# Kernel tuning notes

Hardware: AMD Instinct MI355X
Metric: run time of the kernel (lower is better)

Reference implementation:

```python
import jax, jax.numpy as jnp
import numpy as np

CELL_DIM = 64
FIELD_SIZE = 1.0

def setup_inputs() -> dict:
    key = jax.random.key(0)
    k1, k2 = jax.random.split(key)
    x = jax.random.normal(k1, (8192, CELL_DIM), dtype=jnp.float32)
    placeCells = jax.random.normal(k2, (512, CELL_DIM), dtype=jnp.float32)
    return {"x": x, "placeCells": placeCells}

def reference(x, placeCells):
    # states: (N, cellDim)
    states = x.reshape(-1, CELL_DIM)
    # broadcast L1 distance to every codebook cell: (N, numCells)
    l1 = jnp.sum(jnp.abs(states[:, None, :] - placeCells[None, :, :]), axis=-1)
    dists_squared = l1 * l1
    unnormalized = -dists_squared / (2.0 * FIELD_SIZE * FIELD_SIZE)
    return jax.nn.softmax(unnormalized, axis=1)
```

## Files before the change

### kernel.cpp

```cpp
#include <hip/hip_runtime.h>

#define DIM    64
#define NCELLS 512
#define CHUNK  256
#define KHALF  32
#define ROWS_PER_BLOCK 8
#define NROWS  8192

__global__ __launch_bounds__(256, 4)
void placecells_kernel(const float* __restrict__ x,
                       const float* __restrict__ pc,
                       float* __restrict__ out)
{
    __shared__ float pcT[KHALF * CHUNK];

    const int tid = (int)threadIdx.x;
    const int l   = tid & 63;
    const int w   = __builtin_amdgcn_readfirstlane(tid >> 6);
    const int rowBase = (int)blockIdx.x * ROWS_PER_BLOCK + w * 2;

    float4 a00{0,0,0,0}, a01{0,0,0,0};
    float4 a10{0,0,0,0}, a11{0,0,0,0};

    auto do_phase = [&](int ch, int h, float4& A0, float4& A1) {
        #pragma unroll
        for (int it = 0; it < 8; ++it) {
            int idx = it * 256 + tid;
            int cl  = idx >> 3;
            int kq  = idx & 7;
            float4 v = *(const float4*)(pc + (ch * CHUNK + cl) * DIM + h * KHALF + kq * 4);
            int k4g = h * 8 + kq;
            int pq  = (cl >> 2) ^ k4g;
            float* p = &pcT[(kq * 4) * CHUNK + pq * 4 + (cl & 3)];
            p[0 * CHUNK] = v.x;
            p[1 * CHUNK] = v.y;
            p[2 * CHUNK] = v.z;
            p[3 * CHUNK] = v.w;
        }
        __syncthreads();

        #pragma unroll
        for (int kq = 0; kq < 8; ++kq) {
            const int k4g = h * 8 + kq;
            float4 xv0 = *(const float4*)(x + (rowBase + 0) * DIM + h * KHALF + kq * 4);
            float4 xv1 = *(const float4*)(x + (rowBase + 1) * DIM + h * KHALF + kq * 4);
            const int pq4 = (l ^ k4g) * 4;
            #pragma unroll
            for (int j = 0; j < 4; ++j) {
                float4 pv = *(const float4*)(&pcT[(kq * 4 + j) * CHUNK + pq4]);
                float x0 = (j == 0) ? xv0.x : (j == 1) ? xv0.y : (j == 2) ? xv0.z : xv0.w;
                float x1 = (j == 0) ? xv1.x : (j == 1) ? xv1.y : (j == 2) ? xv1.z : xv1.w;
                A0.x += fabsf(x0 - pv.x); A0.y += fabsf(x0 - pv.y);
                A0.z += fabsf(x0 - pv.z); A0.w += fabsf(x0 - pv.w);
                A1.x += fabsf(x1 - pv.x); A1.y += fabsf(x1 - pv.y);
                A1.z += fabsf(x1 - pv.z); A1.w += fabsf(x1 - pv.w);
            }
        }
        __syncthreads();
    };

    do_phase(0, 0, a00, a10);
    do_phase(0, 1, a00, a10);
    do_phase(1, 0, a01, a11);
    do_phase(1, 1, a01, a11);

    auto finish_row = [&](float4 a, float4 b, int r) {
        float mn = fminf(fminf(fminf(a.x, a.y), fminf(a.z, a.w)),
                         fminf(fminf(b.x, b.y), fminf(b.z, b.w)));
        #pragma unroll
        for (int off = 32; off > 0; off >>= 1)
            mn = fminf(mn, __shfl_xor(mn, off, 64));
        float m2 = mn * mn;

        float e0 = __expf(0.5f * (m2 - a.x * a.x));
        float e1 = __expf(0.5f * (m2 - a.y * a.y));
        float e2 = __expf(0.5f * (m2 - a.z * a.z));
        float e3 = __expf(0.5f * (m2 - a.w * a.w));
        float e4 = __expf(0.5f * (m2 - b.x * b.x));
        float e5 = __expf(0.5f * (m2 - b.y * b.y));
        float e6 = __expf(0.5f * (m2 - b.z * b.z));
        float e7 = __expf(0.5f * (m2 - b.w * b.w));
        float s = ((e0 + e1) + (e2 + e3)) + ((e4 + e5) + (e6 + e7));
        #pragma unroll
        for (int off = 32; off > 0; off >>= 1)
            s += __shfl_xor(s, off, 64);
        float inv = 1.0f / s;

        float* orow = out + (size_t)(rowBase + r) * NCELLS;
        *(float4*)(orow + 4 * l)         = make_float4(e0 * inv, e1 * inv, e2 * inv, e3 * inv);
        *(float4*)(orow + CHUNK + 4 * l) = make_float4(e4 * inv, e5 * inv, e6 * inv, e7 * inv);
    };
    finish_row(a00, a01, 0);
    finish_row(a10, a11, 1);
}

extern "C" void kernel_launch(void* const* d_in, const int* in_sizes, int n_in,
                              void* d_out, int out_size, void* d_ws, size_t ws_size,
                              hipStream_t stream)
{
    const float* x  = (const float*)d_in[0];
    const float* pc = (const float*)d_in[1];
    float* out = (float*)d_out;
    placecells_kernel<<<dim3(NROWS / ROWS_PER_BLOCK), dim3(256), 0, stream>>>(x, pc, out);
}
```

Baseline: 80.37 us.

## Stage the whole place-cell codebook in LDS once per 1024-thread block

Each block now uses 1024 threads covering 32 rows and copies the full 512x64 codebook (128 KB) into dynamic LDS in one transposed, XOR-swizzled pass. This replaces the four chunk/half phases and their extra barriers. The goal is to cut the repeated LDS refills of the codebook per row and the synchronisation between phases. In exchange, the large LDS footprint allows only one block per CU and leaves no overlap between the load and the compute. It also keeps __launch_bounds__(1024,4), which may squeeze the register budget and cause spills.

After: 79.04 us. Within noise of the previous version (-1.6%).

```diff
diff --git a/kernel.cpp b/kernel.cpp
--- a/kernel.cpp
+++ b/kernel.cpp
@@ -2,67 +2,62 @@
 
 #define DIM    64
 #define NCELLS 512
-#define CHUNK  256
-#define KHALF  32
-#define ROWS_PER_BLOCK 8
+#define ROWS_PER_BLOCK 32
 #define NROWS  8192
+#define NBLOCKS (NROWS / ROWS_PER_BLOCK)
 
-__global__ __launch_bounds__(256, 4)
+__global__ __launch_bounds__(1024, 4)
 void placecells_kernel(const float* __restrict__ x,
                        const float* __restrict__ pc,
                        float* __restrict__ out)
 {
-    __shared__ float pcT[KHALF * CHUNK];
+    extern __shared__ float pcT[];
 
     const int tid = (int)threadIdx.x;
     const int l   = tid & 63;
     const int w   = __builtin_amdgcn_readfirstlane(tid >> 6);
     const int rowBase = (int)blockIdx.x * ROWS_PER_BLOCK + w * 2;
 
-    float4 a00{0,0,0,0}, a01{0,0,0,0};
-    float4 a10{0,0,0,0}, a11{0,0,0,0};
+    #pragma unroll
+    for (int it = 0; it < 8; ++it) {
+        int idx = it * 1024 + tid;
+        int cl  = idx >> 4;
+        int kq  = idx & 15;
+        float4 v = *(const float4*)(pc + cl * DIM + kq * 4);
+        int pq = (cl >> 2) ^ kq;
+        float* p = &pcT[(kq * 4) * NCELLS + pq * 4 + (cl & 3)];
+        p[0 * NCELLS] = v.x;
+        p[1 * NCELLS] = v.y;
+        p[2 * NCELLS] = v.z;
+        p[3 * NCELLS] = v.w;
+    }
+    __syncthreads();
 
-    auto do_phase = [&](int ch, int h, float4& A0, float4& A1) {
+    float4 a0A{0,0,0,0}, a0B{0,0,0,0};
+    float4 a1A{0,0,0,0}, a1B{0,0,0,0};
+
+    #pragma unroll 4
+    for (int k4 = 0; k4 < 16; ++k4) {
+        float4 xv0 = *(const float4*)(x + (rowBase + 0) * DIM + k4 * 4);
+        float4 xv1 = *(const float4*)(x + (rowBase + 1) * DIM + k4 * 4);
+        const int pqA = (l ^ k4) * 4;
         #pragma unroll
-        for (int it = 0; it < 8; ++it) {
-            int idx = it * 256 + tid;
-            int cl  = idx >> 3;
-            int kq  = idx & 7;
-            float4 v = *(const float4*)(pc + (ch * CHUNK + cl) * DIM + h * KHALF + kq * 4);
-            int k4g = h * 8 + kq;
-            int pq  = (cl >> 2) ^ k4g;
-            float* p = &pcT[(kq * 4) * CHUNK + pq * 4 + (cl & 3)];
-            p[0 * CHUNK] = v.x;
-            p[1 * CHUNK] = v.y;
-            p[2 * CHUNK] = v.z;
-            p[3 * CHUNK] = v.w;
+        for (int j = 0; j < 4; ++j) {
+            const float* rowp = &pcT[(k4 * 4 + j) * NCELLS];
+            float4 pvA = *(const float4*)(rowp + pqA);
+            float4 pvB = *(const float4*)(rowp + pqA + 256);
+            float x0 = (j == 0) ? xv0.x : (j == 1) ? xv0.y : (j == 2) ? xv0.z : xv0.w;
+            float x1 = (j == 0) ? xv1.x : (j == 1) ? xv1.y : (j == 2) ? xv1.z : xv1.w;
+            a0A.x += fabsf(x0 - pvA.x); a0A.y += fabsf(x0 - pvA.y);
+            a0A.z += fabsf(x0 - pvA.z); a0A.w += fabsf(x0 - pvA.w);
+            a0B.x += fabsf(x0 - pvB.x); a0B.y += fabsf(x0 - pvB.y);
+            a0B.z += fabsf(x0 - pvB.z); a0B.w += fabsf(x0 - pvB.w);
+            a1A.x += fabsf(x1 - pvA.x); a1A.y += fabsf(x1 - pvA.y);
+            a1A.z += fabsf(x1 - pvA.z); a1A.w += fabsf(x1 - pvA.w);
+            a1B.x += fabsf(x1 - pvB.x); a1B.y += fabsf(x1 - pvB.y);
+            a1B.z += fabsf(x1 - pvB.z); a1B.w += fabsf(x1 - pvB.w);
         }
-        __syncthreads();
-
-        #pragma unroll
-        for (int kq = 0; kq < 8; ++kq) {
-            const int k4g = h * 8 + kq;
-            float4 xv0 = *(const float4*)(x + (rowBase + 0) * DIM + h * KHALF + kq * 4);
-            float4 xv1 = *(const float4*)(x + (rowBase + 1) * DIM + h * KHALF + kq * 4);
-            const int pq4 = (l ^ k4g) * 4;
-            #pragma unroll
-            for (int j = 0; j < 4; ++j) {
-                float4 pv = *(const float4*)(&pcT[(kq * 4 + j) * CHUNK + pq4]);
-                float x0 = (j == 0) ? xv0.x : (j == 1) ? xv0.y : (j == 2) ? xv0.z : xv0.w;
-                float x1 = (j == 0) ? xv1.x : (j == 1) ? xv1.y : (j == 2) ? xv1.z : xv1.w;
-                A0.x += fabsf(x0 - pv.x); A0.y += fabsf(x0 - pv.y);
-                A0.z += fabsf(x0 - pv.z); A0.w += fabsf(x0 - pv.w);
-                A1.x += fabsf(x1 - pv.x); A1.y += fabsf(x1 - pv.y);
-                A1.z += fabsf(x1 - pv.z); A1.w += fabsf(x1 - pv.w);
-            }
-        }
-        __syncthreads();
-    };
-
-    do_phase(0, 0, a00, a10);
-    do_phase(0, 1, a00, a10);
-    do_phase(1, 0, a01, a11);
-    do_phase(1, 1, a01, a11);
+    }
 
     auto finish_row = [&](float4 a, float4 b, int r) {
         float mn = fminf(fminf(fminf(a.x, a.y), fminf(a.z, a.w)),
@@ -87,11 +82,11 @@
         float inv = 1.0f / s;
 
         float* orow = out + (size_t)(rowBase + r) * NCELLS;
-        *(float4*)(orow + 4 * l)         = make_float4(e0 * inv, e1 * inv, e2 * inv, e3 * inv);
-        *(float4*)(orow + CHUNK + 4 * l) = make_float4(e4 * inv, e5 * inv, e6 * inv, e7 * inv);
+        *(float4*)(orow + 4 * l)       = make_float4(e0 * inv, e1 * inv, e2 * inv, e3 * inv);
+        *(float4*)(orow + 256 + 4 * l) = make_float4(e4 * inv, e5 * inv, e6 * inv, e7 * inv);
     };
-    finish_row(a00, a01, 0);
-    finish_row(a10, a11, 1);
+    finish_row(a0A, a0B, 0);
+    finish_row(a1A, a1B, 1);
 }
 
 extern "C" void kernel_launch(void* const* d_in, const int* in_sizes, int n_in,
@@ -101,5 +96,5 @@
     const float* x  = (const float*)d_in[0];
     const float* pc = (const float*)d_in[1];
     float* out = (float*)d_out;
-    placecells_kernel<<<dim3(NROWS / ROWS_PER_BLOCK), dim3(256), 0, stream>>>(x, pc, out);
+    placecells_kernel<<<dim3(NBLOCKS), dim3(1024), DIM * NCELLS * sizeof(float), stream>>>(x, pc, out);
 }
```
